# Kernel tuning notes

Measured on AMD Instinct MI355X. Metric: run time of the kernel, lower is better.

## Reference

```python
import jax, jax.numpy as jnp
import numpy as np

SIGMA = 0.5
ALPHA = 1.0  # current_iter = 0 -> cosine annealing returns alpha_max
KSIZE = 5
B, C, H, W, NBOX = 16, 256, 80, 80, 32


def _gaussian_kernel():
    # matches torch: arange(-5//2+1, 5//2+1) = [-2,-1,0,1,2]
    ax = jnp.arange(-(KSIZE // 2), KSIZE // 2 + 1, dtype=jnp.float32)
    xx, yy = jnp.meshgrid(ax, ax, indexing='ij')
    k = jnp.exp(-(xx ** 2 + yy ** 2) / (2.0 * SIGMA ** 2))
    return (k / k.sum())[None, None]  # [1,1,5,5] OIHW


def setup_inputs() -> dict:
    key = jax.random.key(0)
    k1, k2 = jax.random.split(key)
    x = jax.random.normal(k1, (B, C, H, W), dtype=jnp.float32)
    # normalized xywh boxes in [0,1] (code path box.max() <= 1.0)
    boxes = jax.random.uniform(k2, (B, NBOX, 4), dtype=jnp.float32)
    return {"x": x, "boxes": boxes, "kernel": _gaussian_kernel()}


def _attention_map(boxes, height, width):
    # Vectorized rasterization of all boxes at once (torch loops per box).
    xc, yc, bw, bh = boxes[..., 0], boxes[..., 1], boxes[..., 2], boxes[..., 3]
    # int() truncates toward zero -> jnp.trunc; then clamp as in torch code
    x1 = jnp.maximum(0.0, jnp.trunc((xc - bw / 2) * width)).astype(jnp.int32)
    y1 = jnp.maximum(0.0, jnp.trunc((yc - bh / 2) * height)).astype(jnp.int32)
    x2 = jnp.minimum(float(width - 1), jnp.trunc((xc + bw / 2) * width)).astype(jnp.int32)
    y2 = jnp.minimum(float(height - 1), jnp.trunc((yc + bh / 2) * height)).astype(jnp.int32)
    valid = (x2 > x1) & (y2 > y1)  # [B, N]
    rows = jnp.arange(height, dtype=jnp.int32)[None, None, :, None]  # [1,1,H,1]
    cols = jnp.arange(width, dtype=jnp.int32)[None, None, None, :]   # [1,1,1,W]
    inside = ((rows >= y1[:, :, None, None]) & (rows <= y2[:, :, None, None]) &
              (cols >= x1[:, :, None, None]) & (cols <= x2[:, :, None, None]) &
              valid[:, :, None, None])  # [B,N,H,W]
    mask = jnp.any(inside, axis=1).astype(jnp.float32)  # union over boxes -> [B,H,W]
    return mask[:, None]  # [B,1,H,W]


def _smooth(att, kernel):
    pad = KSIZE // 2
    att = jnp.pad(att, ((0, 0), (0, 0), (pad, pad), (pad, pad)), mode='reflect')
    return jax.lax.conv_general_dilated(
        att, kernel, window_strides=(1, 1), padding='VALID',
        dimension_numbers=('NCHW', 'OIHW', 'NCHW'))


def reference(x, boxes, kernel):
    _, _, height, width = x.shape
    att = _attention_map(boxes, height, width)      # [B,1,H,W]
    att = _smooth(att, kernel)                      # gaussian smoothing (sigma>0)
    return x + ALPHA * att * x                      # broadcast over channels
```

## Files before the change

### kernel.cpp

```cpp
#include <hip/hip_runtime.h>


namespace {
constexpr int kB = 16;
constexpr int kC = 256;
constexpr int kH = 80;
constexpr int kW = 80;
constexpr int kNBox = 32;
constexpr float kAlpha = 1.0f;
constexpr int kHW = kH * kW;
constexpr int kHW4 = kHW / 4;
constexpr int kBF4 = kC * kHW4;
constexpr size_t kWsNeed = (size_t)kB * kHW * sizeof(float);

__device__ __forceinline__ int reflect_idx(int r, int n) {
    return r < 0 ? -r : (r > n - 1 ? 2 * (n - 1) - r : r);
}
}

__global__ __launch_bounds__(256) void ae_rasterize_kernel(
    const float* __restrict__ boxes,
    const float* __restrict__ gk,
    float* __restrict__ fac)
{
    __shared__ int sx1[kNBox], sy1[kNBox], sx2[kNBox], sy2[kNBox];
    __shared__ float sk[25];
    __shared__ float smask[kH][kW];

    const int b = blockIdx.x;
    const int t = threadIdx.x;

    if (t < kNBox) {
        const float* bp = boxes + (size_t)(b * kNBox + t) * 4;
        float xc = bp[0], yc = bp[1], bw = bp[2], bh = bp[3];
        float fx1 = fmaxf(0.0f, truncf((xc - bw * 0.5f) * (float)kW));
        float fy1 = fmaxf(0.0f, truncf((yc - bh * 0.5f) * (float)kH));
        float fx2 = fminf((float)(kW - 1), truncf((xc + bw * 0.5f) * (float)kW));
        float fy2 = fminf((float)(kH - 1), truncf((yc + bh * 0.5f) * (float)kH));
        int ix1 = (int)fx1, iy1 = (int)fy1, ix2 = (int)fx2, iy2 = (int)fy2;
        bool valid = (ix2 > ix1) && (iy2 > iy1);
        sx1[t] = ix1;
        sx2[t] = ix2;
        sy1[t] = valid ? iy1 : 1;
        sy2[t] = valid ? iy2 : 0;
    } else if (t >= 64 && t < 64 + 25) {
        sk[t - 64] = gk[t - 64];
    }
    __syncthreads();

    for (int p = t; p < kHW; p += 256) {
        int h = p / kW, w = p % kW;
        float m = 0.0f;
#pragma unroll
        for (int n = 0; n < kNBox; ++n) {
            bool in = (h >= sy1[n]) && (h <= sy2[n]) && (w >= sx1[n]) && (w <= sx2[n]);
            m = in ? 1.0f : m;
        }
        smask[h][w] = m;
    }
    __syncthreads();

    for (int p = t; p < kHW; p += 256) {
        int h = p / kW, w = p % kW;
        float acc = 0.0f;
#pragma unroll
        for (int i = 0; i < 5; ++i) {
            int rr = reflect_idx(h + i - 2, kH);
#pragma unroll
            for (int j = 0; j < 5; ++j) {
                int cc = reflect_idx(w + j - 2, kW);
                acc += sk[i * 5 + j] * smask[rr][cc];
            }
        }
        fac[(size_t)b * kHW + p] = 1.0f + kAlpha * acc;
    }
}

__global__ __launch_bounds__(256) void ae_stream_kernel(
    const float4* __restrict__ x4,
    const float4* __restrict__ fac4,
    float4* __restrict__ o4)
{
    const int blk = blockIdx.x;
    const int b = blk / 200;
    const int off = (blk % 200) * 256 + threadIdx.x;
    const float4 f = fac4[b * kHW4 + (off % kHW4)];
    const size_t base = (size_t)b * kBF4 + off;
#pragma unroll
    for (int k = 0; k < 8; ++k) {
        size_t idx = base + (size_t)k * 51200;
        float4 v = x4[idx];
        v.x *= f.x;
        v.y *= f.y;
        v.z *= f.z;
        v.w *= f.w;
        o4[idx] = v;
    }
}

__global__ __launch_bounds__(320) void ae_fused_kernel(
    const float* __restrict__ x,
    const float* __restrict__ boxes,
    const float* __restrict__ gk,
    float* __restrict__ out)
{
    __shared__ int sx1[kNBox], sy1[kNBox], sx2[kNBox], sy2[kNBox];
    __shared__ float sk[25];
    __shared__ float smask[5][kW];
    __shared__ __attribute__((aligned(16))) float sfac[kW];

    const int b = blockIdx.x / kH;
    const int h = blockIdx.x % kH;
    const int t = threadIdx.x;

    if (t < kNBox) {
        const float* bp = boxes + (size_t)(b * kNBox + t) * 4;
        float xc = bp[0], yc = bp[1], bw = bp[2], bh = bp[3];
        float fx1 = fmaxf(0.0f, truncf((xc - bw * 0.5f) * (float)kW));
        float fy1 = fmaxf(0.0f, truncf((yc - bh * 0.5f) * (float)kH));
        float fx2 = fminf((float)(kW - 1), truncf((xc + bw * 0.5f) * (float)kW));
        float fy2 = fminf((float)(kH - 1), truncf((yc + bh * 0.5f) * (float)kH));
        int ix1 = (int)fx1, iy1 = (int)fy1, ix2 = (int)fx2, iy2 = (int)fy2;
        bool valid = (ix2 > ix1) && (iy2 > iy1);
        sx1[t] = ix1;
        sx2[t] = ix2;
        sy1[t] = valid ? iy1 : 1;
        sy2[t] = valid ? iy2 : 0;
    } else if (t >= 64 && t < 64 + 25) {
        sk[t - 64] = gk[t - 64];
    }
    __syncthreads();

    for (int p = t; p < 5 * kW; p += 320) {
        int i = p / kW, c = p % kW;
        int rr = reflect_idx(h + i - 2, kH);
        float m = 0.0f;
#pragma unroll
        for (int n = 0; n < kNBox; ++n) {
            bool in = (rr >= sy1[n]) && (rr <= sy2[n]) && (c >= sx1[n]) && (c <= sx2[n]);
            m = in ? 1.0f : m;
        }
        smask[i][c] = m;
    }
    __syncthreads();

    if (t < kW) {
        float acc = 0.0f;
#pragma unroll
        for (int i = 0; i < 5; ++i) {
#pragma unroll
            for (int j = 0; j < 5; ++j) {
                int cc = reflect_idx(t + j - 2, kW);
                acc += sk[i * 5 + j] * smask[i][cc];
            }
        }
        sfac[t] = 1.0f + kAlpha * acc;
    }
    __syncthreads();

    const int j = t % 20;
    const int c0 = t / 20;
    const float4 f4 = *reinterpret_cast<const float4*>(&sfac[j * 4]);
    const size_t rowbase = (size_t)b * (kC * kH * kW / 4) + (size_t)h * (kW / 4);
    const float4* x4 = reinterpret_cast<const float4*>(x) + rowbase;
    float4* o4 = reinterpret_cast<float4*>(out) + rowbase;
#pragma unroll
    for (int it = 0; it < kC / 16; ++it) {
        int c = c0 + it * 16;
        size_t off = (size_t)c * (kH * kW / 4) + j;
        float4 v = x4[off];
        v.x *= f4.x;
        v.y *= f4.y;
        v.z *= f4.z;
        v.w *= f4.w;
        o4[off] = v;
    }
}

extern "C" void kernel_launch(void* const* d_in, const int* in_sizes, int n_in,
                              void* d_out, int out_size, void* d_ws, size_t ws_size,
                              hipStream_t stream) {
    const float* x     = (const float*)d_in[0];
    const float* boxes = (const float*)d_in[1];
    const float* gk    = (const float*)d_in[2];
    float* out         = (float*)d_out;

    if (ws_size >= kWsNeed) {
        float* fac = (float*)d_ws;
        ae_rasterize_kernel<<<dim3(kB), dim3(256), 0, stream>>>(boxes, gk, fac);
        ae_stream_kernel<<<dim3(kB * 200), dim3(256), 0, stream>>>(
            (const float4*)x, (const float4*)fac, (float4*)out);
    } else {
        ae_fused_kernel<<<dim3(kB * kH), dim3(320), 0, stream>>>(x, boxes, gk, out);
    }
}
```

Measured before the change: 229.1 us.

## Split rasterize across row bands and batch loads with nontemporal stores

The rasterize kernel now runs one block per 8-row band (10 bands per batch) with a 12-row mask halo, instead of one block per batch. This raises parallelism from 16 blocks to 160 and shortens this serial prologue. The stream kernel issues all 8 loads before any multiplies and writes the output with nontemporal stores to reduce cache pollution. Halo rows are rasterized redundantly, which adds a small amount of compute.

New measurement: 192.2 us. -16.1%, faster.

```diff
diff --git a/kernel.cpp b/kernel.cpp
--- a/kernel.cpp
+++ b/kernel.cpp
@@ -13,6 +13,8 @@
 constexpr int kBF4 = kC * kHW4;
 constexpr size_t kWsNeed = (size_t)kB * kHW * sizeof(float);
 
+typedef float vfloat4 __attribute__((ext_vector_type(4)));
+
 __device__ __forceinline__ int reflect_idx(int r, int n) {
     return r < 0 ? -r : (r > n - 1 ? 2 * (n - 1) - r : r);
 }
@@ -25,9 +27,10 @@
 {
     __shared__ int sx1[kNBox], sy1[kNBox], sx2[kNBox], sy2[kNBox];
     __shared__ float sk[25];
-    __shared__ float smask[kH][kW];
-
-    const int b = blockIdx.x;
+    __shared__ float smask[12][kW];
+
+    const int b = blockIdx.x / 10;
+    const int h0 = (blockIdx.x % 10) * 8;
     const int t = threadIdx.x;
 
     if (t < kNBox) {
@@ -48,53 +51,54 @@
     }
     __syncthreads();
 
-    for (int p = t; p < kHW; p += 256) {
-        int h = p / kW, w = p % kW;
+    for (int p = t; p < 12 * kW; p += 256) {
+        int lr = p / kW, w = p % kW;
+        int h = reflect_idx(h0 - 2 + lr, kH);
         float m = 0.0f;
 #pragma unroll
         for (int n = 0; n < kNBox; ++n) {
             bool in = (h >= sy1[n]) && (h <= sy2[n]) && (w >= sx1[n]) && (w <= sx2[n]);
             m = in ? 1.0f : m;
         }
-        smask[h][w] = m;
-    }
-    __syncthreads();
-
-    for (int p = t; p < kHW; p += 256) {
-        int h = p / kW, w = p % kW;
+        smask[lr][w] = m;
+    }
+    __syncthreads();
+
+    for (int p = t; p < 8 * kW; p += 256) {
+        int r = p / kW, w = p % kW;
         float acc = 0.0f;
 #pragma unroll
         for (int i = 0; i < 5; ++i) {
-            int rr = reflect_idx(h + i - 2, kH);
 #pragma unroll
             for (int j = 0; j < 5; ++j) {
                 int cc = reflect_idx(w + j - 2, kW);
-                acc += sk[i * 5 + j] * smask[rr][cc];
+                acc += sk[i * 5 + j] * smask[r + i][cc];
             }
         }
-        fac[(size_t)b * kHW + p] = 1.0f + kAlpha * acc;
+        fac[(size_t)b * kHW + (size_t)(h0 + r) * kW + w] = 1.0f + kAlpha * acc;
     }
 }
 
 __global__ __launch_bounds__(256) void ae_stream_kernel(
-    const float4* __restrict__ x4,
-    const float4* __restrict__ fac4,
-    float4* __restrict__ o4)
+    const vfloat4* __restrict__ x4,
+    const vfloat4* __restrict__ fac4,
+    vfloat4* __restrict__ o4)
 {
     const int blk = blockIdx.x;
     const int b = blk / 200;
     const int off = (blk % 200) * 256 + threadIdx.x;
-    const float4 f = fac4[b * kHW4 + (off % kHW4)];
+    const vfloat4 f = fac4[b * kHW4 + (off % kHW4)];
     const size_t base = (size_t)b * kBF4 + off;
+
+    vfloat4 v[8];
 #pragma unroll
     for (int k = 0; k < 8; ++k) {
-        size_t idx = base + (size_t)k * 51200;
-        float4 v = x4[idx];
-        v.x *= f.x;
-        v.y *= f.y;
-        v.z *= f.z;
-        v.w *= f.w;
-        o4[idx] = v;
+        v[k] = x4[base + (size_t)k * 51200];
+    }
+#pragma unroll
+    for (int k = 0; k < 8; ++k) {
+        vfloat4 w = v[k] * f;
+        __builtin_nontemporal_store(w, &o4[base + (size_t)k * 51200]);
     }
 }
 
@@ -187,9 +191,9 @@
 
     if (ws_size >= kWsNeed) {
         float* fac = (float*)d_ws;
-        ae_rasterize_kernel<<<dim3(kB), dim3(256), 0, stream>>>(boxes, gk, fac);
+        ae_rasterize_kernel<<<dim3(kB * 10), dim3(256), 0, stream>>>(boxes, gk, fac);
         ae_stream_kernel<<<dim3(kB * 200), dim3(256), 0, stream>>>(
-            (const float4*)x, (const float4*)fac, (float4*)out);
+            (const vfloat4*)x, (const vfloat4*)fac, (vfloat4*)out);
     } else {
         ae_fused_kernel<<<dim3(kB * kH), dim3(320), 0, stream>>>(x, boxes, gk, out);
     }
```
